# Performance work log

Measured on AMD Instinct MI355X. Metric: run time of the kernel, lower is better.

## Reference

```python
import jax, jax.numpy as jnp
import numpy as np

N_NODES = 100000
D = 128        # input_dim / feature dim
H = 128        # hidden_dim
O = 64         # output_dim (classes)
B = 4096       # batch of seed nodes
S = 16         # sample_num (neighbor fan-out)


def setup_inputs() -> dict:
    key = jax.random.key(0)
    k1, k2, k3, k4, k5, k6, k7 = jax.random.split(key, 7)
    nodes = jax.random.randint(k1, (B,), 0, N_NODES)
    neighbors_1 = jax.random.randint(k2, (B, S), 0, N_NODES)
    neighbors_2 = jax.random.randint(k3, (B * S, S), 0, N_NODES)
    node_features = jax.random.normal(k4, (N_NODES, D), dtype=jnp.float32)
    # xavier-uniform, no bias (matches nn.Linear weight layout [out, in])
    def xavier(k, out_d, in_d):
        lim = float(np.sqrt(6.0 / (in_d + out_d)))
        return jax.random.uniform(k, (out_d, in_d), jnp.float32, -lim, lim)
    W1 = xavier(k5, H, 2 * D)   # fc_layer_1 (concat=True -> input_dim*2)
    W2 = xavier(k6, H, 2 * D)   # fc_layer_2
    Wo = xavier(k7, O, H)       # output_layer
    return {"nodes": nodes, "neighbors_1": neighbors_1, "neighbors_2": neighbors_2,
            "node_features": node_features, "W1": W1, "W2": W2, "Wo": Wo}


def reference(nodes, neighbors_1, neighbors_2, node_features, W1, W2, Wo):
    # Level-1 neighbor node list (flattened samples of the seed nodes)
    neighs_nodes_1 = neighbors_1.reshape(-1)                 # [B*S]
    features_origin = node_features[nodes]                   # [B, D]
    features_1 = node_features[neighs_nodes_1]               # [B*S, D]

    # aggregator_1: mean over sampled 2-hop neighbors of each level-1 node
    agg_feat_1 = node_features[neighbors_2].mean(axis=1)     # [B*S, D]
    agg_feat_1 = jnp.concatenate([features_1, agg_feat_1], axis=-1)  # [B*S, 2D]
    agg_embed_1 = jax.nn.relu(agg_feat_1 @ W1.T)             # [B*S, H] (unused downstream, as in original)

    # aggregator_2: mean over sampled 1-hop neighbors of each seed node
    agg_feat_2 = node_features[neighbors_1].mean(axis=1)     # [B, D]
    agg_feat_2 = jnp.concatenate([features_origin, agg_feat_2], axis=-1)  # [B, 2D]
    agg_embed_2 = jax.nn.relu(agg_feat_2 @ W2.T)             # [B, H]

    logits = agg_embed_2 @ Wo.T                              # [B, O]
    return jax.nn.softmax(logits, axis=-1)
```

## Files before the change

kernel.cpp:

```cpp
#include <hip/hip_runtime.h>


constexpr int D = 128;
constexpr int H = 128;
constexpr int O = 64;
constexpr int S = 16;
constexpr int NB = 4096;
constexpr int SPB = 8;
constexpr int THREADS = 256;

__global__ __launch_bounds__(THREADS, 2) void sage_fused(
    const int* __restrict__ nodes,
    const int* __restrict__ neighbors_1,
    const float* __restrict__ node_features,
    const float* __restrict__ W2,
    const float* __restrict__ Wo,
    float* __restrict__ out)
{
    __shared__ float cat[SPB][2 * D];
    __shared__ float part[THREADS][SPB + 1];
    __shared__ float h[SPB][H];
    __shared__ int   nbs[SPB][S];
    __shared__ int   sid[SPB];

    const int t = threadIdx.x;
    const int seed0 = blockIdx.x * SPB;

    if (t < SPB) sid[t] = nodes[seed0 + t];
    if (t < SPB * S) nbs[t / S][t % S] = neighbors_1[seed0 * S + t];
    __syncthreads();

    {
        const int d4 = t & 31;
        const int r  = t >> 5;
        const float4* nf = reinterpret_cast<const float4*>(node_features);
        float4 sum = make_float4(0.f, 0.f, 0.f, 0.f);
        #pragma unroll
        for (int s = 0; s < S; ++s) {
            const float4 v = nf[(size_t)nbs[r][s] * (D / 4) + d4];
            sum.x += v.x; sum.y += v.y; sum.z += v.z; sum.w += v.w;
        }
        const float4 org = nf[(size_t)sid[r] * (D / 4) + d4];
        *reinterpret_cast<float4*>(&cat[r][4 * d4]) = org;
        const float4 mean = make_float4(sum.x * (1.f / 16.f), sum.y * (1.f / 16.f),
                                        sum.z * (1.f / 16.f), sum.w * (1.f / 16.f));
        *reinterpret_cast<float4*>(&cat[r][D + 4 * d4]) = mean;
    }
    __syncthreads();

    {
        const int j = t & (H - 1);
        const int half = t >> 7;
        const float* w = W2 + (size_t)j * (2 * D) + half * D;
        const float* c0 = &cat[0][half * D];
        float acc[SPB];
        #pragma unroll
        for (int r = 0; r < SPB; ++r) acc[r] = 0.f;
        for (int k = 0; k < D; k += 4) {
            const float4 wv = *reinterpret_cast<const float4*>(w + k);
            #pragma unroll
            for (int r = 0; r < SPB; ++r) {
                const float* c = c0 + r * (2 * D) + k;
                acc[r] = fmaf(wv.x, c[0], acc[r]);
                acc[r] = fmaf(wv.y, c[1], acc[r]);
                acc[r] = fmaf(wv.z, c[2], acc[r]);
                acc[r] = fmaf(wv.w, c[3], acc[r]);
            }
        }
        #pragma unroll
        for (int r = 0; r < SPB; ++r) part[t][r] = acc[r];
    }
    __syncthreads();

    for (int i = t; i < SPB * H; i += THREADS) {
        const int r = i >> 7;
        const int j = i & (H - 1);
        const float v = part[j][r] + part[j + H][r];
        h[r][j] = v > 0.f ? v : 0.f;
    }
    __syncthreads();

    {
        const int lane = t & 63;
        const int wv_id = t >> 6;
        const float* wo = Wo + (size_t)lane * H;
        for (int r = wv_id; r < SPB; r += 4) {
            float acc = 0.f;
            #pragma unroll
            for (int k = 0; k < H; k += 4) {
                const float4 wv = *reinterpret_cast<const float4*>(wo + k);
                acc = fmaf(wv.x, h[r][k + 0], acc);
                acc = fmaf(wv.y, h[r][k + 1], acc);
                acc = fmaf(wv.z, h[r][k + 2], acc);
                acc = fmaf(wv.w, h[r][k + 3], acc);
            }
            float m = acc;
            #pragma unroll
            for (int off = 32; off >= 1; off >>= 1)
                m = fmaxf(m, __shfl_xor(m, off));
            const float e = __expf(acc - m);
            float ssum = e;
            #pragma unroll
            for (int off = 32; off >= 1; off >>= 1)
                ssum += __shfl_xor(ssum, off);
            out[(size_t)(seed0 + r) * O + lane] = e / ssum;
        }
    }
}

extern "C" void kernel_launch(void* const* d_in, const int* in_sizes, int n_in,
                              void* d_out, int out_size, void* d_ws, size_t ws_size,
                              hipStream_t stream) {
    const int*   nodes         = (const int*)d_in[0];
    const int*   neighbors_1   = (const int*)d_in[1];
    const float* node_features = (const float*)d_in[3];
    const float* W2            = (const float*)d_in[5];
    const float* Wo            = (const float*)d_in[6];
    float*       out           = (float*)d_out;

    sage_fused<<<NB / SPB, THREADS, 0, stream>>>(
        nodes, neighbors_1, node_features, W2, Wo, out);
}
```

Baseline: 113.8 us.

## Halve seeds per block, split neighbor gather across wave halves, remap GEMV work

Seeds per block drop from 8 to 4, so twice as many blocks launch and the occupancy hint rises to 4. Each wave now handles one seed. Its two 32-lane halves each gather 8 neighbors and combine them with a cross-lane shuffle, and neighbor ids are read straight from global memory as int4 instead of staged in shared memory. The W2 GEMV is remapped so each thread computes two output columns over a quarter of K, with a 4-way reduction afterwards. The aim is more memory-level parallelism for the random gathers and fewer barriers, at the cost of reloading W2 from cache twice as often per seed.

```diff
diff --git a/kernel.cpp b/kernel.cpp
--- a/kernel.cpp
+++ b/kernel.cpp
@@ -6,10 +6,10 @@
 constexpr int O = 64;
 constexpr int S = 16;
 constexpr int NB = 4096;
-constexpr int SPB = 8;
+constexpr int SPB = 4;
 constexpr int THREADS = 256;
 
-__global__ __launch_bounds__(THREADS, 2) void sage_fused(
+__global__ __launch_bounds__(THREADS, 4) void sage_fused(
     const int* __restrict__ nodes,
     const int* __restrict__ neighbors_1,
     const float* __restrict__ node_features,
@@ -18,93 +18,117 @@
     float* __restrict__ out)
 {
     __shared__ float cat[SPB][2 * D];
-    __shared__ float part[THREADS][SPB + 1];
+    __shared__ float part[THREADS][9];
     __shared__ float h[SPB][H];
-    __shared__ int   nbs[SPB][S];
-    __shared__ int   sid[SPB];
 
     const int t = threadIdx.x;
     const int seed0 = blockIdx.x * SPB;
 
-    if (t < SPB) sid[t] = nodes[seed0 + t];
-    if (t < SPB * S) nbs[t / S][t % S] = neighbors_1[seed0 * S + t];
-    __syncthreads();
+    {
+        const int lane = t & 63;
+        const int r    = __builtin_amdgcn_readfirstlane(t >> 6);
+        const int d4   = lane & 31;
+        const int sub  = lane >> 5;
+        const float4* nf = reinterpret_cast<const float4*>(node_features);
 
-    {
-        const int d4 = t & 31;
-        const int r  = t >> 5;
-        const float4* nf = reinterpret_cast<const float4*>(node_features);
+        const int4* nbp = reinterpret_cast<const int4*>(
+            neighbors_1 + (size_t)(seed0 + r) * S + sub * 8);
+        const int4 n0 = nbp[0];
+        const int4 n1 = nbp[1];
+
         float4 sum = make_float4(0.f, 0.f, 0.f, 0.f);
+        const int ids[8] = {n0.x, n0.y, n0.z, n0.w, n1.x, n1.y, n1.z, n1.w};
         #pragma unroll
-        for (int s = 0; s < S; ++s) {
-            const float4 v = nf[(size_t)nbs[r][s] * (D / 4) + d4];
+        for (int s = 0; s < 8; ++s) {
+            const float4 v = nf[(size_t)ids[s] * (D / 4) + d4];
             sum.x += v.x; sum.y += v.y; sum.z += v.z; sum.w += v.w;
         }
-        const float4 org = nf[(size_t)sid[r] * (D / 4) + d4];
-        *reinterpret_cast<float4*>(&cat[r][4 * d4]) = org;
-        const float4 mean = make_float4(sum.x * (1.f / 16.f), sum.y * (1.f / 16.f),
-                                        sum.z * (1.f / 16.f), sum.w * (1.f / 16.f));
-        *reinterpret_cast<float4*>(&cat[r][D + 4 * d4]) = mean;
+        float4 tot;
+        tot.x = sum.x + __shfl_xor(sum.x, 32);
+        tot.y = sum.y + __shfl_xor(sum.y, 32);
+        tot.z = sum.z + __shfl_xor(sum.z, 32);
+        tot.w = sum.w + __shfl_xor(sum.w, 32);
+
+        if (sub == 0) {
+            const int org = nodes[seed0 + r];
+            const float4 ov = nf[(size_t)org * (D / 4) + d4];
+            *reinterpret_cast<float4*>(&cat[r][4 * d4]) = ov;
+        } else {
+            const float4 mean = make_float4(tot.x * (1.f / 16.f), tot.y * (1.f / 16.f),
+                                            tot.z * (1.f / 16.f), tot.w * (1.f / 16.f));
+            *reinterpret_cast<float4*>(&cat[r][D + 4 * d4]) = mean;
+        }
     }
     __syncthreads();
 
     {
-        const int j = t & (H - 1);
-        const int half = t >> 7;
-        const float* w = W2 + (size_t)j * (2 * D) + half * D;
-        const float* c0 = &cat[0][half * D];
-        float acc[SPB];
+        const int j0 = t & 63;
+        const int q  = t >> 6;
+        const float* w0 = W2 + (size_t)j0 * (2 * D) + q * 64;
+        const float* w1 = W2 + (size_t)(j0 + 64) * (2 * D) + q * 64;
+        float acc[SPB][2];
         #pragma unroll
-        for (int r = 0; r < SPB; ++r) acc[r] = 0.f;
-        for (int k = 0; k < D; k += 4) {
-            const float4 wv = *reinterpret_cast<const float4*>(w + k);
+        for (int r = 0; r < SPB; ++r) { acc[r][0] = 0.f; acc[r][1] = 0.f; }
+
+        for (int k = 0; k < 64; k += 4) {
+            const float4 a0 = *reinterpret_cast<const float4*>(w0 + k);
+            const float4 a1 = *reinterpret_cast<const float4*>(w1 + k);
             #pragma unroll
             for (int r = 0; r < SPB; ++r) {
-                const float* c = c0 + r * (2 * D) + k;
-                acc[r] = fmaf(wv.x, c[0], acc[r]);
-                acc[r] = fmaf(wv.y, c[1], acc[r]);
-                acc[r] = fmaf(wv.z, c[2], acc[r]);
-                acc[r] = fmaf(wv.w, c[3], acc[r]);
+                const float4 c = *reinterpret_cast<const float4*>(&cat[r][q * 64 + k]);
+                acc[r][0] = fmaf(a0.x, c.x, acc[r][0]);
+                acc[r][0] = fmaf(a0.y, c.y, acc[r][0]);
+                acc[r][0] = fmaf(a0.z, c.z, acc[r][0]);
+                acc[r][0] = fmaf(a0.w, c.w, acc[r][0]);
+                acc[r][1] = fmaf(a1.x, c.x, acc[r][1]);
+                acc[r][1] = fmaf(a1.y, c.y, acc[r][1]);
+                acc[r][1] = fmaf(a1.z, c.z, acc[r][1]);
+                acc[r][1] = fmaf(a1.w, c.w, acc[r][1]);
             }
         }
         #pragma unroll
-        for (int r = 0; r < SPB; ++r) part[t][r] = acc[r];
+        for (int r = 0; r < SPB; ++r) {
+            part[t][r * 2 + 0] = acc[r][0];
+            part[t][r * 2 + 1] = acc[r][1];
+        }
     }
     __syncthreads();
 
     for (int i = t; i < SPB * H; i += THREADS) {
-        const int r = i >> 7;
-        const int j = i & (H - 1);
-        const float v = part[j][r] + part[j + H][r];
+        const int r  = i >> 7;
+        const int j  = i & (H - 1);
+        const int jj = j >> 6;
+        const int j0 = j & 63;
+        float v = 0.f;
+        #pragma unroll
+        for (int q = 0; q < 4; ++q) v += part[(q << 6) | j0][r * 2 + jj];
         h[r][j] = v > 0.f ? v : 0.f;
     }
     __syncthreads();
 
     {
         const int lane = t & 63;
-        const int wv_id = t >> 6;
+        const int r    = t >> 6;
         const float* wo = Wo + (size_t)lane * H;
-        for (int r = wv_id; r < SPB; r += 4) {
-            float acc = 0.f;
-            #pragma unroll
-            for (int k = 0; k < H; k += 4) {
-                const float4 wv = *reinterpret_cast<const float4*>(wo + k);
-                acc = fmaf(wv.x, h[r][k + 0], acc);
-                acc = fmaf(wv.y, h[r][k + 1], acc);
-                acc = fmaf(wv.z, h[r][k + 2], acc);
-                acc = fmaf(wv.w, h[r][k + 3], acc);
-            }
-            float m = acc;
-            #pragma unroll
-            for (int off = 32; off >= 1; off >>= 1)
-                m = fmaxf(m, __shfl_xor(m, off));
-            const float e = __expf(acc - m);
-            float ssum = e;
-            #pragma unroll
-            for (int off = 32; off >= 1; off >>= 1)
-                ssum += __shfl_xor(ssum, off);
-            out[(size_t)(seed0 + r) * O + lane] = e / ssum;
+        float acc = 0.f;
+        #pragma unroll
+        for (int k = 0; k < H; k += 4) {
+            const float4 wv = *reinterpret_cast<const float4*>(wo + k);
+            acc = fmaf(wv.x, h[r][k + 0], acc);
+            acc = fmaf(wv.y, h[r][k + 1], acc);
+            acc = fmaf(wv.z, h[r][k + 2], acc);
+            acc = fmaf(wv.w, h[r][k + 3], acc);
         }
+        float m = acc;
+        #pragma unroll
+        for (int off = 32; off >= 1; off >>= 1)
+            m = fmaxf(m, __shfl_xor(m, off));
+        const float e = __expf(acc - m);
+        float ssum = e;
+        #pragma unroll
+        for (int off = 32; off >= 1; off >>= 1)
+            ssum += __shfl_xor(ssum, off);
+        out[(size_t)(seed0 + r) * O + lane] = e / ssum;
     }
 }
 
```

After: 138.4 us. +21.6%, slower.
